# Performance work log

Measured on AMD Instinct MI355X. Metric: run time of the kernel, lower is better.

## Reference

```python
import jax, jax.numpy as jnp
import numpy as np

TEMPERATURE = 0.1
GAMMA = 0.5
LOSS_WEIGHT = 1.0
LINE_CLASS = 2
COS_EPS = 1e-8      # torch F.cosine_similarity eps
RADIUS = 1.0        # positive-pair spatial radius
SELF_EPS = 1e-6     # excludes self pairs (dist ~ 0) from positives
NCE_EPS = 1e-6


def _pairwise_dist(coords):
    # Euclidean cdist [N, N] with a sqrt that is safe at 0 (self pairs)
    sq = jnp.sum(coords * coords, axis=1)
    d2 = jnp.maximum(sq[:, None] + sq[None, :] - 2.0 * (coords @ coords.T), 0.0)
    safe = jnp.where(d2 > 0.0, d2, 1.0)
    return jnp.where(d2 > 0.0, jnp.sqrt(safe), 0.0)


def setup_inputs() -> dict:
    key = jax.random.key(0)
    k1, k2, k3 = jax.random.split(key, 3)
    N, D = 4096, 64
    features = jax.random.normal(k1, (N, D), dtype=jnp.float32)
    # uniform in a 10x10x10 box -> ~30 neighbors within radius 1.0 per point
    coords = jax.random.uniform(k2, (N, 3), dtype=jnp.float32) * 10.0
    labels = jax.random.randint(k3, (N,), 0, 3)  # class 2 == power line
    return {"features": features, "labels": labels, "coords": coords}


def reference(features, labels, coords):
    # Static-shape equivalent of boolean-indexing the line-class points:
    # weight w_i = 1 iff labels[i] == LINE_CLASS. All sums / means below are
    # restricted to line points via w, matching torch masked gather exactly.
    w = (labels == LINE_CLASS).astype(features.dtype)        # [N]
    M = jnp.sum(w)                                           # number of line points
    pair_w = w[:, None] * w[None, :]                         # [N, N]

    # cosine similarity matrix  [N, N]
    norms = jnp.maximum(jnp.linalg.norm(features, axis=1, keepdims=True), COS_EPS)
    fn = features / norms
    feat_sim = fn @ fn.T

    # spatial distance matrix and pos / neg pair masks  [N, N]
    coord_dist = _pairwise_dist(coords)
    pos_raw = ((coord_dist < RADIUS) & (coord_dist > SELF_EPS)).astype(features.dtype)
    pos_w = pair_w * pos_raw
    neg_w = pair_w * (1.0 - pos_raw)   # ~pos_mask within line subset (incl. self)

    # InfoNCE over line points
    exp_sim = jnp.exp(feat_sim / TEMPERATURE)
    pos_sum = jnp.sum(exp_sim * pos_w, axis=1)               # [N]
    neg_sum = jnp.sum(exp_sim * neg_w, axis=1)               # [N]
    ratio = pos_sum / (neg_sum + pos_sum + NCE_EPS)
    per_point = -jnp.log(jnp.where(w > 0, ratio, 1.0))       # 0 for non-line pts
    info_nce = jnp.sum(per_point) / M                        # mean over line pts

    # continuity: mean over the M x M line-pair block
    feat_dist = 1.0 - feat_sim
    continuity = jnp.sum(jnp.abs(feat_dist - coord_dist) * pos_w) / (M * M)

    return (info_nce + GAMMA * continuity) * LOSS_WEIGHT
```

## Files before the change

### kernel.cpp

```cpp
#include <hip/hip_runtime.h>
#include <hip/hip_bf16.h>

#define LINE_CLASS 2
#define NJ 32

__global__ __launch_bounds__(256) void prep_kernel(const float* __restrict__ feat,
                                                   const int* __restrict__ labels,
                                                   const float* __restrict__ coords,
                                                   int N,
                                                   int* __restrict__ idx,
                                                   int* __restrict__ Mp,
                                                   float* __restrict__ fnAll,
                                                   float4* __restrict__ cAll) {
    const int tid = threadIdx.x;

    if (blockIdx.x == 0) {
        __shared__ int scnt[256];
        const int EPT = (N + 255) / 256;
        const int i0  = tid * EPT;
        unsigned long long bits = 0ull;
        for (int u = 0; u < EPT; ++u) {
            const int i = i0 + u;
            if (i < N && labels[i] == LINE_CLASS) bits |= (1ull << u);
        }
        const int cnt = __popcll(bits);
        scnt[tid] = cnt;
        __syncthreads();
        for (int s = 1; s < 256; s <<= 1) {
            int v = scnt[tid];
            if (tid >= s) v += scnt[tid - s];
            __syncthreads();
            scnt[tid] = v;
            __syncthreads();
        }
        int pos = scnt[tid] - cnt;
        for (int u = 0; u < EPT; ++u) {
            if (bits & (1ull << u)) idx[pos++] = i0 + u;
        }
        if (tid == 255) *Mp = scnt[255];
        return;
    }

    const int i = (blockIdx.x - 1) * 4 + (tid >> 6);
    const int d = tid & 63;
    if (i >= N) return;
    const float v = feat[(size_t)i * 64 + d];
    float ss = v * v;
    #pragma unroll
    for (int off = 32; off > 0; off >>= 1) ss += __shfl_xor(ss, off);
    const float dn = fmaxf(sqrtf(ss), 1e-8f);
    fnAll[(size_t)i * 64 + d] = v / dn;
    if (d == 0) {
        const float x = coords[i * 3 + 0];
        const float y = coords[i * 3 + 1];
        const float z = coords[i * 3 + 2];
        cAll[i] = make_float4(x, y, z, fmaf(x, x, fmaf(y, y, z * z)));
    }
}

__global__ __launch_bounds__(256) void pair_kernel(const float* __restrict__ fnAll,
                                                   const float4* __restrict__ cAll,
                                                   const int* __restrict__ idx,
                                                   const int* __restrict__ Mp,
                                                   int N,
                                                   float* __restrict__ posp,
                                                   float* __restrict__ negp,
                                                   float* __restrict__ contp) {
    const int b   = blockIdx.x;
    const int js  = blockIdx.y;
    const int tid = threadIdx.x;
    const int r   = tid & 63;
    const int q   = tid >> 6;
    const int M   = *Mp;
    const int own0 = b * 64;
    const int k    = own0 + r;

    if (own0 >= M) return;
    const bool valid = (k < M);

    const int chunk = (M + NJ - 1) / NJ;
    const int j0   = js * chunk;
    const int j1   = (j0 + chunk < M) ? (j0 + chunk) : M;
    const int jcnt = j1 - j0;

    __shared__ float sp[4][64], sn[4][64], sc[256];

    if (jcnt <= 0) {
        if (q == 0 && valid) {
            posp[(size_t)js * N + k] = 0.0f;
            negp[(size_t)js * N + k] = 0.0f;
        }
        if (tid == 0) contp[b * NJ + js] = 0.0f;
        return;
    }

    float4 f4[16];
    float4 ci;
    if (valid) {
        const int i = idx[k];
        const float4* fr = (const float4*)(fnAll + (size_t)i * 64);
        #pragma unroll
        for (int t = 0; t < 16; ++t) f4[t] = fr[t];
        ci = cAll[i];
    } else {
        #pragma unroll
        for (int t = 0; t < 16; ++t) f4[t] = make_float4(0.f, 0.f, 0.f, 0.f);
        ci = make_float4(0.f, 0.f, 0.f, 0.f);
    }

    float pos_s = 0.0f, neg_s = 0.0f, cont_s = 0.0f;
    for (int j = j0 + q; j < j1; j += 4) {
        const int ju = __builtin_amdgcn_readfirstlane(j);
        const int ij = idx[ju];
        const float4* __restrict__ fjv = (const float4*)(fnAll + (size_t)ij * 64);
        float dot = 0.0f;
        #pragma unroll
        for (int t = 0; t < 16; ++t) {
            const float4 bv = fjv[t];
            dot = fmaf(f4[t].x, bv.x, dot);
            dot = fmaf(f4[t].y, bv.y, dot);
            dot = fmaf(f4[t].z, bv.z, dot);
            dot = fmaf(f4[t].w, bv.w, dot);
        }
        const float4 cj = cAll[ij];
        const float cdot = fmaf(ci.x, cj.x, fmaf(ci.y, cj.y, ci.z * cj.z));
        const float d2 = fmaxf(ci.w + cj.w - 2.0f * cdot, 0.0f);
        const float dist = (d2 > 0.0f) ? sqrtf(d2) : 0.0f;
        const float e = expf(dot * 10.0f);
        const bool isPos = (dist < 1.0f) && (dist > 1e-6f);
        if (isPos) {
            pos_s += e;
            if (valid) cont_s += fabsf((1.0f - dot) - dist);
        } else {
            neg_s += e;
        }
    }

    sp[q][r] = pos_s;
    sn[q][r] = neg_s;
    sc[tid]  = cont_s;
    __syncthreads();
    if (q == 0 && valid) {
        posp[(size_t)js * N + k] = sp[0][r] + sp[1][r] + sp[2][r] + sp[3][r];
        negp[(size_t)js * N + k] = sn[0][r] + sn[1][r] + sn[2][r] + sn[3][r];
    }
    for (int s = 128; s > 0; s >>= 1) {
        if (tid < s) sc[tid] += sc[tid + s];
        __syncthreads();
    }
    if (tid == 0) contp[b * NJ + js] = sc[0];
}

__global__ __launch_bounds__(1024) void final_kernel(const float* __restrict__ posp,
                                                     const float* __restrict__ negp,
                                                     const float* __restrict__ contp,
                                                     const int* __restrict__ Mp,
                                                     int N,
                                                     float* __restrict__ out) {
    const int tid = threadIdx.x;
    const int M = *Mp;
    float nce = 0.0f;
    for (int k = tid; k < M; k += 1024) {
        float P = 0.0f, Ng = 0.0f;
        #pragma unroll
        for (int js = 0; js < NJ; ++js) {
            P  += posp[(size_t)js * N + k];
            Ng += negp[(size_t)js * N + k];
        }
        const float ratio = fmaxf(P / (Ng + P + 1e-6f), 1e-38f);
        nce += -logf(ratio);
    }
    float cont = 0.0f;
    const int nact = (M + 63) / 64;
    const int nslots = nact * NJ;
    for (int c = tid; c < nslots; c += 1024) cont += contp[c];

    __shared__ float r1[1024];
    __shared__ float r2[1024];
    r1[tid] = nce;
    r2[tid] = cont;
    __syncthreads();
    for (int s = 512; s > 0; s >>= 1) {
        if (tid < s) { r1[tid] += r1[tid + s]; r2[tid] += r2[tid + s]; }
        __syncthreads();
    }
    if (tid == 0) {
        const float Mf = (float)M;
        out[0] = (r1[0] / Mf + 0.5f * (r2[0] / (Mf * Mf))) * 1.0f;
    }
}

extern "C" void kernel_launch(void* const* d_in, const int* in_sizes, int n_in,
                              void* d_out, int out_size, void* d_ws, size_t ws_size,
                              hipStream_t stream) {
    const float* feat   = (const float*)d_in[0];
    const int*   labels = (const int*)  d_in[1];
    const float* coords = (const float*)d_in[2];
    const int N = in_sizes[1];

    char* ws = (char*)d_ws;
    int*    Mp    = (int*)   (ws + 0);
    int*    idx   = (int*)   (ws + 1024);
    float4* cAll  = (float4*)(ws + 32768);
    float*  fnAll = (float*) (ws + 131072);
    float*  posp  = (float*) (ws + 2097152);
    float*  negp  = (float*) (ws + 2621440);
    float*  contp = (float*) (ws + 3145728);

    const int NB = (N + 63) / 64;

    prep_kernel<<<1 + (N + 3) / 4, 256, 0, stream>>>(feat, labels, coords, N,
                                                     idx, Mp, fnAll, cAll);
    pair_kernel<<<dim3(NB, NJ), 256, 0, stream>>>(fnAll, cAll, idx, Mp, N,
                                                  posp, negp, contp);
    final_kernel<<<1, 1024, 0, stream>>>(posp, negp, contp, Mp, N, (float*)d_out);
}
```

Baseline: 88.05 us.

## Drop normalized feature buffer, apply inverse norms in pair kernel

The prep kernel no longer writes a normalized copy of the features. It stores each row's inverse norm in the w slot of the coordinate float4, and the pair kernel scales the raw dot product by the two inverse norms. Distances are computed from coordinate differences, and the positive-pair test compares squared distance, so sqrt only runs for positive pairs. Other changes: a fast __expf, four independent dot accumulators, vectorized label loads, and prep blocks that handle 16 rows each. This removes a 1 MB write/read round trip and some ALU work. It risks small numerical differences from __expf and the changed distance formula.

Result: no change. 88.81 us (+0.9%).

```diff
diff --git a/kernel.cpp b/kernel.cpp
--- a/kernel.cpp
+++ b/kernel.cpp
@@ -1,5 +1,4 @@
 #include <hip/hip_runtime.h>
-#include <hip/hip_bf16.h>
 
 #define LINE_CLASS 2
 #define NJ 32
@@ -10,7 +9,6 @@
                                                    int N,
                                                    int* __restrict__ idx,
                                                    int* __restrict__ Mp,
-                                                   float* __restrict__ fnAll,
                                                    float4* __restrict__ cAll) {
     const int tid = threadIdx.x;
 
@@ -19,9 +17,20 @@
         const int EPT = (N + 255) / 256;
         const int i0  = tid * EPT;
         unsigned long long bits = 0ull;
-        for (int u = 0; u < EPT; ++u) {
-            const int i = i0 + u;
-            if (i < N && labels[i] == LINE_CLASS) bits |= (1ull << u);
+        if ((EPT & 3) == 0 && i0 + EPT <= N) {
+            const int4* lv = (const int4*)(labels + i0);
+            for (int u4 = 0; u4 < EPT / 4; ++u4) {
+                const int4 l4 = lv[u4];
+                if (l4.x == LINE_CLASS) bits |= 1ull << (u4 * 4 + 0);
+                if (l4.y == LINE_CLASS) bits |= 1ull << (u4 * 4 + 1);
+                if (l4.z == LINE_CLASS) bits |= 1ull << (u4 * 4 + 2);
+                if (l4.w == LINE_CLASS) bits |= 1ull << (u4 * 4 + 3);
+            }
+        } else {
+            for (int u = 0; u < EPT; ++u) {
+                const int i = i0 + u;
+                if (i < N && labels[i] == LINE_CLASS) bits |= (1ull << u);
+            }
         }
         const int cnt = __popcll(bits);
         scnt[tid] = cnt;
@@ -41,24 +50,23 @@
         return;
     }
 
-    const int i = (blockIdx.x - 1) * 4 + (tid >> 6);
-    const int d = tid & 63;
-    if (i >= N) return;
-    const float v = feat[(size_t)i * 64 + d];
-    float ss = v * v;
+    const int l   = tid & 63;
+    const int row = (blockIdx.x - 1) * 16 + (tid >> 6) * 4 + (l >> 4);
+    const int l16 = l & 15;
+    if (row >= N) return;
+    const float4 v = *(const float4*)(feat + (size_t)row * 64 + l16 * 4);
+    float ss = fmaf(v.x, v.x, fmaf(v.y, v.y, fmaf(v.z, v.z, v.w * v.w)));
     #pragma unroll
-    for (int off = 32; off > 0; off >>= 1) ss += __shfl_xor(ss, off);
-    const float dn = fmaxf(sqrtf(ss), 1e-8f);
-    fnAll[(size_t)i * 64 + d] = v / dn;
-    if (d == 0) {
-        const float x = coords[i * 3 + 0];
-        const float y = coords[i * 3 + 1];
-        const float z = coords[i * 3 + 2];
-        cAll[i] = make_float4(x, y, z, fmaf(x, x, fmaf(y, y, z * z)));
-    }
-}
-
-__global__ __launch_bounds__(256) void pair_kernel(const float* __restrict__ fnAll,
+    for (int off = 8; off > 0; off >>= 1) ss += __shfl_xor(ss, off);
+    if (l16 == 0) {
+        const float inv = 1.0f / fmaxf(sqrtf(ss), 1e-8f);
+        cAll[row] = make_float4(coords[row * 3 + 0],
+                                coords[row * 3 + 1],
+                                coords[row * 3 + 2], inv);
+    }
+}
+
+__global__ __launch_bounds__(256) void pair_kernel(const float* __restrict__ feat,
                                                    const float4* __restrict__ cAll,
                                                    const int* __restrict__ idx,
                                                    const int* __restrict__ Mp,
@@ -98,7 +106,7 @@
     float4 ci;
     if (valid) {
         const int i = idx[k];
-        const float4* fr = (const float4*)(fnAll + (size_t)i * 64);
+        const float4* fr = (const float4*)(feat + (size_t)i * 64);
         #pragma unroll
         for (int t = 0; t < 16; ++t) f4[t] = fr[t];
         ci = cAll[i];
@@ -112,25 +120,43 @@
     for (int j = j0 + q; j < j1; j += 4) {
         const int ju = __builtin_amdgcn_readfirstlane(j);
         const int ij = idx[ju];
-        const float4* __restrict__ fjv = (const float4*)(fnAll + (size_t)ij * 64);
-        float dot = 0.0f;
-        #pragma unroll
-        for (int t = 0; t < 16; ++t) {
-            const float4 bv = fjv[t];
-            dot = fmaf(f4[t].x, bv.x, dot);
-            dot = fmaf(f4[t].y, bv.y, dot);
-            dot = fmaf(f4[t].z, bv.z, dot);
-            dot = fmaf(f4[t].w, bv.w, dot);
-        }
+        const float4* __restrict__ fjv = (const float4*)(feat + (size_t)ij * 64);
+        float dot0 = 0.0f, dot1 = 0.0f, dot2 = 0.0f, dot3 = 0.0f;
+        #pragma unroll
+        for (int t = 0; t < 16; t += 4) {
+            const float4 b0 = fjv[t + 0];
+            dot0 = fmaf(f4[t + 0].x, b0.x, dot0);
+            dot0 = fmaf(f4[t + 0].y, b0.y, dot0);
+            dot0 = fmaf(f4[t + 0].z, b0.z, dot0);
+            dot0 = fmaf(f4[t + 0].w, b0.w, dot0);
+            const float4 b1 = fjv[t + 1];
+            dot1 = fmaf(f4[t + 1].x, b1.x, dot1);
+            dot1 = fmaf(f4[t + 1].y, b1.y, dot1);
+            dot1 = fmaf(f4[t + 1].z, b1.z, dot1);
+            dot1 = fmaf(f4[t + 1].w, b1.w, dot1);
+            const float4 b2 = fjv[t + 2];
+            dot2 = fmaf(f4[t + 2].x, b2.x, dot2);
+            dot2 = fmaf(f4[t + 2].y, b2.y, dot2);
+            dot2 = fmaf(f4[t + 2].z, b2.z, dot2);
+            dot2 = fmaf(f4[t + 2].w, b2.w, dot2);
+            const float4 b3 = fjv[t + 3];
+            dot3 = fmaf(f4[t + 3].x, b3.x, dot3);
+            dot3 = fmaf(f4[t + 3].y, b3.y, dot3);
+            dot3 = fmaf(f4[t + 3].z, b3.z, dot3);
+            dot3 = fmaf(f4[t + 3].w, b3.w, dot3);
+        }
+        const float dot = (dot0 + dot1) + (dot2 + dot3);
         const float4 cj = cAll[ij];
-        const float cdot = fmaf(ci.x, cj.x, fmaf(ci.y, cj.y, ci.z * cj.z));
-        const float d2 = fmaxf(ci.w + cj.w - 2.0f * cdot, 0.0f);
-        const float dist = (d2 > 0.0f) ? sqrtf(d2) : 0.0f;
-        const float e = expf(dot * 10.0f);
-        const bool isPos = (dist < 1.0f) && (dist > 1e-6f);
+        const float sim = dot * (ci.w * cj.w);
+        const float dx = ci.x - cj.x;
+        const float dy = ci.y - cj.y;
+        const float dz = ci.z - cj.z;
+        const float d2 = fmaf(dx, dx, fmaf(dy, dy, dz * dz));
+        const float e = __expf(sim * 10.0f);
+        const bool isPos = (d2 < 1.0f) && (d2 > 1e-12f);
         if (isPos) {
             pos_s += e;
-            if (valid) cont_s += fabsf((1.0f - dot) - dist);
+            if (valid) cont_s += fabsf((1.0f - sim) - sqrtf(d2));
         } else {
             neg_s += e;
         }
@@ -202,16 +228,15 @@
     int*    Mp    = (int*)   (ws + 0);
     int*    idx   = (int*)   (ws + 1024);
     float4* cAll  = (float4*)(ws + 32768);
-    float*  fnAll = (float*) (ws + 131072);
-    float*  posp  = (float*) (ws + 2097152);
-    float*  negp  = (float*) (ws + 2621440);
-    float*  contp = (float*) (ws + 3145728);
+    float*  posp  = (float*) (ws + 131072);
+    float*  negp  = (float*) (ws + 655360);
+    float*  contp = (float*) (ws + 1179648);
 
     const int NB = (N + 63) / 64;
 
-    prep_kernel<<<1 + (N + 3) / 4, 256, 0, stream>>>(feat, labels, coords, N,
-                                                     idx, Mp, fnAll, cAll);
-    pair_kernel<<<dim3(NB, NJ), 256, 0, stream>>>(fnAll, cAll, idx, Mp, N,
+    prep_kernel<<<1 + (N + 15) / 16, 256, 0, stream>>>(feat, labels, coords, N,
+                                                       idx, Mp, cAll);
+    pair_kernel<<<dim3(NB, NJ), 256, 0, stream>>>(feat, cAll, idx, Mp, N,
                                                   posp, negp, contp);
     final_kernel<<<1, 1024, 0, stream>>>(posp, negp, contp, Mp, N, (float*)d_out);
 }
```
